# Optimization experiments

Measured on AMD Instinct MI355X. Metric: run time of the kernel, lower is better.

## Reference

```python
import jax, jax.numpy as jnp
import numpy as np

B, T, D_IN, D_OUT = 16, 2048, 2048, 2048
N_ADAPTERS, RANK = 8, 16


def setup_inputs() -> dict:
    key = jax.random.key(0)
    k_x, k_w, k_a, k_b, k_s, k_idx = jax.random.split(key, 6)
    x = jax.random.normal(k_x, (B, T, D_IN), dtype=jnp.float32)
    # frozen base weight (nn.Linear stores W as (d_out, d_in)); bias=False
    W = jax.random.normal(k_w, (D_OUT, D_IN), dtype=jnp.float32) * (1.0 / np.sqrt(D_IN))
    # stacked adapter bank: A[a] is (r, d_in), Bm[a] is (d_out, r)
    A = jax.random.normal(k_a, (N_ADAPTERS, RANK, D_IN), dtype=jnp.float32) * 0.02
    Bm = jax.random.normal(k_b, (N_ADAPTERS, D_OUT, RANK), dtype=jnp.float32) * 0.02
    scalings = jnp.ones((N_ADAPTERS,), dtype=jnp.float32)  # alpha / r, pre-merged
    adapter_idx = jax.random.randint(k_idx, (B,), 0, N_ADAPTERS, dtype=jnp.int32)
    return {"x": x, "W": W, "A": A, "Bm": Bm, "scalings": scalings,
            "adapter_idx": adapter_idx}


def reference(x, W, A, Bm, scalings, adapter_idx):
    # base path: H = x @ W^T   -> (B, T, d_out)
    H = jnp.einsum("btd,od->bto", x, W)
    # per-request adapter gather (replaces the Python loop over adapter groups)
    A_b = A[adapter_idx]          # (B, r, d_in)
    B_b = Bm[adapter_idx]         # (B, d_out, r)
    s_b = scalings[adapter_idx]   # (B,)
    # low-rank delta: (x @ A^T) @ B^T, done per request, fully batched
    xa = jnp.einsum("btd,brd->btr", x, A_b)        # (B, T, r)
    delta = jnp.einsum("btr,bor->bto", xa, B_b)    # (B, T, d_out)
    # original computes delta under torch.no_grad() with detached A/B
    delta = jax.lax.stop_gradient(delta * s_b[:, None, None])
    return H + delta
```

## Files before the change

### kernel.cpp

```cpp
#include <hip/hip_runtime.h>
#include <stdint.h>

typedef unsigned short u16;
typedef __attribute__((ext_vector_type(4))) short s16x4;
typedef __attribute__((ext_vector_type(8))) short short8;
typedef __attribute__((ext_vector_type(4))) float f32x4;

static __device__ __forceinline__ u16 f2bf(float f) {
    union { float f; uint32_t u; } c; c.f = f;
    uint32_t u = c.u;
    u += 0x7FFFu + ((u >> 16) & 1u);
    return (u16)(u >> 16);
}

#define D_IN   2048
#define D_OUT  2048
#define MTOT   32768
#define BK     64
#define NTM    32

__device__ __forceinline__ void gload16(const u16* g, u16* l) {
    __builtin_amdgcn_global_load_lds(
        (const __attribute__((address_space(1))) void*)g,
        (__attribute__((address_space(3))) void*)l, 16, 0, 0);
}

__global__ __launch_bounds__(256) void k_prep(
    const float* __restrict__ W, const float* __restrict__ A, const float* __restrict__ Bm,
    u16* __restrict__ Wb, u16* __restrict__ Ap, u16* __restrict__ Bp)
{
    const int b = blockIdx.x, tid = threadIdx.x;
    if (b < 2048) {
        int i = (b * 256 + tid) * 8;
        const float4* p = (const float4*)(W + i);
        float4 v0 = p[0], v1 = p[1];
        short8 o;
        o[0]=f2bf(v0.x); o[1]=f2bf(v0.y); o[2]=f2bf(v0.z); o[3]=f2bf(v0.w);
        o[4]=f2bf(v1.x); o[5]=f2bf(v1.y); o[6]=f2bf(v1.z); o[7]=f2bf(v1.w);
        *(short8*)(Wb + i) = o;
    } else if (b < 6144) {
        int i = (b - 2048) * 256 + tid;
        int d = i & 2047, r = (i >> 11) & 63, a = i >> 17;
        Ap[i] = (r < 16) ? f2bf(A[(((a << 4) + r) << 11) + d]) : (u16)0;
    } else {
        int i = (b - 6144) * 256 + tid;
        int j = i & 63, n = (i >> 6) & 2047, a = i >> 17;
        Bp[i] = (j < 16) ? f2bf(Bm[((((a << 11) + n)) << 4) + j]) : (u16)0;
    }
}

__global__ __launch_bounds__(256) void k_cast_x_xa(
    const float* __restrict__ x, const u16* __restrict__ Ap,
    const float* __restrict__ scal, const int* __restrict__ aidx,
    u16* __restrict__ xb, u16* __restrict__ xa)
{
    __shared__ __align__(16) u16 Xs[128 * BK];
    __shared__ __align__(16) u16 Ps[64 * BK];
    const int tid = threadIdx.x, lane = tid & 63, wid = tid >> 6;
    const int m0 = blockIdx.x << 7;
    const int a = aidx[m0 >> 11];
    const float s = scal[a];
    const int wr = wid >> 1, wc = wid & 1;
    const int arow = (wr << 6) + (lane & 15);
    const int brow = (wc << 5) + (lane & 15);
    const int scol = ((lane & 7) ^ (lane >> 3)) << 3;

    f32x4 acc[4][2];
    #pragma unroll
    for (int i = 0; i < 4; ++i) { acc[i][0] = 0.f; acc[i][1] = 0.f; }

    const int xrow_l = tid >> 4;
    const int xcol   = (tid & 15) << 2;
    const int wslot  = (tid & 15) >> 1;
    const int wsub   = (tid & 1) << 2;

    const u16* apg = Ap + ((size_t)a << 17);
    const u16* gP[2]; u16* lP[2];
    #pragma unroll
    for (int it = 0; it < 2; ++it) {
        const int chunk = (wid << 1) + it;
        const int row = (chunk << 3) + (lane >> 3);
        gP[it] = apg + ((size_t)row << 11) + scol;
        lP[it] = Ps + (chunk << 9) + (lane << 3);
    }

    for (int kt = 0; kt < NTM; ++kt) {
        const int k0 = kt << 6;
        float4 xv[8];
        #pragma unroll
        for (int r = 0; r < 8; ++r)
            xv[r] = *(const float4*)(x + ((size_t)(m0 + (r << 4) + xrow_l) << 11) + k0 + xcol);
        #pragma unroll
        for (int r = 0; r < 8; ++r) {
            const int row = (r << 4) + xrow_l;
            s16x4 c4;
            c4[0]=f2bf(xv[r].x); c4[1]=f2bf(xv[r].y); c4[2]=f2bf(xv[r].z); c4[3]=f2bf(xv[r].w);
            *(s16x4*)(Xs + (row << 6) + ((wslot ^ (row & 7)) << 3) + wsub) = c4;
            *(s16x4*)(xb + ((size_t)(m0 + row) << 11) + k0 + xcol) = c4;
        }
        gload16(gP[0] + k0, lP[0]);
        gload16(gP[1] + k0, lP[1]);
        asm volatile("s_waitcnt vmcnt(0)" ::: "memory");
        __syncthreads();
        #pragma unroll
        for (int kk = 0; kk < 2; ++kk) {
            const int sl = ((kk << 2) + (lane >> 4)) ^ (lane & 7);
            short8 af[4], bv[2];
            #pragma unroll
            for (int mi = 0; mi < 4; ++mi)
                af[mi] = *(const short8*)(Xs + ((arow + mi * 16) << 6) + (sl << 3));
            #pragma unroll
            for (int ni = 0; ni < 2; ++ni)
                bv[ni] = *(const short8*)(Ps + ((brow + ni * 16) << 6) + (sl << 3));
            #pragma unroll
            for (int mi = 0; mi < 4; ++mi)
                #pragma unroll
                for (int ni = 0; ni < 2; ++ni)
                    acc[mi][ni] = __builtin_amdgcn_mfma_f32_16x16x32_bf16(af[mi], bv[ni], acc[mi][ni], 0, 0, 0);
        }
        __syncthreads();
    }

    #pragma unroll
    for (int mi = 0; mi < 4; ++mi) {
        #pragma unroll
        for (int ni = 0; ni < 2; ++ni) {
            const int cc = (wc << 5) + ni * 16 + (lane & 15);
            #pragma unroll
            for (int rr = 0; rr < 4; ++rr) {
                const int mm = m0 + (wr << 6) + mi * 16 + ((lane >> 4) << 2) + rr;
                xa[((size_t)mm << 6) + cc] = f2bf(acc[mi][ni][rr] * s);
            }
        }
    }
}

__global__ __launch_bounds__(512, 2) void k_gemm(
    const u16* __restrict__ xb, const u16* __restrict__ Wb,
    const u16* __restrict__ xa, const u16* __restrict__ Bp,
    const int* __restrict__ aidx, float* __restrict__ out)
{
    __shared__ __align__(16) u16 LDS[2 * 32768];
    const int tid = threadIdx.x, lane = tid & 63, wid = tid >> 6;

    const int newbid = (blockIdx.x & 7) * 128 + (blockIdx.x >> 3);
    const int bm = newbid >> 3, bn = newbid & 7;
    const int m0 = bm << 8, n0 = bn << 8;
    const int wr = wid >> 2, wc = wid & 3;
    const int a = aidx[m0 >> 11];

    f32x4 acc[8][4];
    #pragma unroll
    for (int i = 0; i < 8; ++i)
        #pragma unroll
        for (int j = 0; j < 4; ++j) acc[i][j] = 0.0f;

    const int sc = ((tid & 7) ^ ((tid >> 3) & 7)) << 3;
    const int srw = tid >> 3;

    const int sl0 = (((lane >> 4)    ) ^ (lane & 7)) << 3;
    const int sl1 = (((lane >> 4) + 4) ^ (lane & 7)) << 3;
    const int aRowBase = (wr << 7) + (lane & 15);
    const int bRowBase = (wc << 6) + (lane & 15);

    short8 af[4][2], bv[4][2];

    auto STG = [&](const u16* ptr, int stride, int rowbase, int kofs, int ldsofs) {
        const u16* s_ = ptr + ((size_t)(rowbase + srw)) * stride + kofs + sc;
        gload16(s_,                          &LDS[ldsofs + (tid << 3)]);
        gload16(s_ + ((size_t)stride << 6),  &LDS[ldsofs + 4096 + (tid << 3)]);
    };
    auto SA = [&](int tt, int h) {
        const int lo = ((tt & 1) << 15) + (h << 13);
        if (tt < NTM) STG(xb, 2048, m0 + (h << 7), tt << 6, lo);
        else          STG(xa, 64,   m0 + (h << 7), 0,       lo);
    };
    auto SB = [&](int tt, int h) {
        const int lo = ((tt & 1) << 15) + 16384 + (h << 13);
        if (tt < NTM) STG(Wb, 2048, n0 + (h << 7), tt << 6, lo);
        else          STG(Bp, 64,   (a << 11) + n0 + (h << 7), 0, lo);
    };

    #define BAR  __builtin_amdgcn_s_barrier()

    #define RDA(c_, mq_) do { _Pragma("unroll")                                     \
        for (int mi = 0; mi < 4; ++mi) {                                            \
            const int row = aRowBase + ((mq_) << 6) + (mi << 4);                    \
            af[mi][0] = *(const short8*)&LDS[((c_) << 15) + (row << 6) + sl0];      \
            af[mi][1] = *(const short8*)&LDS[((c_) << 15) + (row << 6) + sl1];      \
        } } while (0)

    #define RDB(c_, ni_) do {                                                       \
            const int row = bRowBase + ((ni_) << 4);                                \
            bv[ni_][0] = *(const short8*)&LDS[((c_) << 15) + 16384 + (row << 6) + sl0]; \
            bv[ni_][1] = *(const short8*)&LDS[((c_) << 15) + 16384 + (row << 6) + sl1]; \
        } while (0)

    #define MM(mq_, ns_) do { _Pragma("unroll")                                     \
        for (int kk = 0; kk < 2; ++kk) _Pragma("unroll")                            \
        for (int mi = 0; mi < 4; ++mi) _Pragma("unroll")                            \
        for (int j = 0; j < 2; ++j)                                                 \
            acc[(mq_) * 4 + mi][(ns_) * 2 + j] =                                    \
                __builtin_amdgcn_mfma_f32_16x16x32_bf16(af[mi][kk],                 \
                    bv[(ns_) * 2 + j][kk], acc[(mq_) * 4 + mi][(ns_) * 2 + j], 0, 0, 0); \
        } while (0)

    SA(0, 0); SA(0, 1); SB(0, 0); SB(0, 1);

    for (int t = 0; t <= NTM; ++t) {
        const int c = t & 1;
        if (t < NTM) { SA(t + 1, 0); SA(t + 1, 1); SB(t + 1, 0); SB(t + 1, 1); }
        if (t < NTM) asm volatile("s_waitcnt vmcnt(8)" ::: "memory");
        else         asm volatile("s_waitcnt vmcnt(0)" ::: "memory");
        BAR;
        RDB(c, 0); RDB(c, 1); RDA(c, 0);
        MM(0, 0);
        RDB(c, 2); RDB(c, 3);
        MM(0, 1);
        RDA(c, 1);
        MM(1, 0);
        MM(1, 1);
        BAR;
    }

    #undef MM
    #undef RDB
    #undef RDA
    #undef BAR

    #pragma unroll
    for (int mi = 0; mi < 8; ++mi) {
        #pragma unroll
        for (int ni = 0; ni < 4; ++ni) {
            const int nn = n0 + (wc << 6) + ni * 16 + (lane & 15);
            #pragma unroll
            for (int r = 0; r < 4; ++r) {
                const int mm = m0 + (wr << 7) + mi * 16 + ((lane >> 4) << 2) + r;
                out[((size_t)mm << 11) + nn] = acc[mi][ni][r];
            }
        }
    }
}

extern "C" void kernel_launch(void* const* d_in, const int* in_sizes, int n_in,
                              void* d_out, int out_size, void* d_ws, size_t ws_size,
                              hipStream_t stream) {
    const float* x  = (const float*)d_in[0];
    const float* W  = (const float*)d_in[1];
    const float* A  = (const float*)d_in[2];
    const float* Bm = (const float*)d_in[3];
    const float* sc = (const float*)d_in[4];
    const int* aidx = (const int*)d_in[5];
    float* out = (float*)d_out;

    char* ws = (char*)d_ws;
    u16* xb = (u16*)(ws);
    u16* Wb = (u16*)(ws + 134217728);
    u16* Ap = (u16*)(ws + 134217728 + 8388608);
    u16* Bp = (u16*)(ws + 134217728 + 8388608 + 2097152);
    u16* xa = (u16*)(ws + 134217728 + 8388608 + 2097152 + 2097152);

    hipLaunchKernelGGL(k_prep,      dim3(10240), dim3(256), 0, stream, W, A, Bm, Wb, Ap, Bp);
    hipLaunchKernelGGL(k_cast_x_xa, dim3(256),   dim3(256), 0, stream, x, Ap, sc, aidx, xb, xa);
    hipLaunchKernelGGL(k_gemm,      dim3(1024),  dim3(512), 0, stream, xb, Wb, xa, Bp, aidx, out);
}
```

Before: 396.9 us.

## Switch GEMM to 32x32x16 MFMA with fragment-packed operand layouts

```diff
diff --git a/kernel.cpp b/kernel.cpp
--- a/kernel.cpp
+++ b/kernel.cpp
@@ -5,6 +5,7 @@
 typedef __attribute__((ext_vector_type(4))) short s16x4;
 typedef __attribute__((ext_vector_type(8))) short short8;
 typedef __attribute__((ext_vector_type(4))) float f32x4;
+typedef __attribute__((ext_vector_type(16))) float f32x16;
 
 static __device__ __forceinline__ u16 f2bf(float f) {
     union { float f; uint32_t u; } c; c.f = f;
@@ -18,6 +19,7 @@
 #define MTOT   32768
 #define BK     64
 #define NTM    32
+
 
 __device__ __forceinline__ void gload16(const u16* g, u16* l) {
     __builtin_amdgcn_global_load_lds(
@@ -32,12 +34,15 @@
     const int b = blockIdx.x, tid = threadIdx.x;
     if (b < 2048) {
         int i = (b * 256 + tid) * 8;
+        int n = i >> 11, c = i & 2047;
         const float4* p = (const float4*)(W + i);
         float4 v0 = p[0], v1 = p[1];
         short8 o;
         o[0]=f2bf(v0.x); o[1]=f2bf(v0.y); o[2]=f2bf(v0.z); o[3]=f2bf(v0.w);
         o[4]=f2bf(v1.x); o[5]=f2bf(v1.y); o[6]=f2bf(v1.z); o[7]=f2bf(v1.w);
-        *(short8*)(Wb + i) = o;
+        const int np = n >> 8, kt = c >> 6, nb = (n & 255) >> 5, ks = (c >> 4) & 3;
+        const int lane = (n & 31) + (((c >> 3) & 1) << 5);
+        *(short8*)(Wb + (((size_t)(np << 5) + kt) << 14) + (((nb << 2) + ks) << 9) + (lane << 3)) = o;
     } else if (b < 6144) {
         int i = (b - 2048) * 256 + tid;
         int d = i & 2047, r = (i >> 11) & 63, a = i >> 17;
@@ -45,7 +50,10 @@
     } else {
         int i = (b - 6144) * 256 + tid;
         int j = i & 63, n = (i >> 6) & 2047, a = i >> 17;
-        Bp[i] = (j < 16) ? f2bf(Bm[((((a << 11) + n)) << 4) + j]) : (u16)0;
+        float v = (j < 16) ? Bm[((((a << 11) + n)) << 4) + j] : 0.0f;
+        const int np = n >> 8, nb = (n & 255) >> 5, ks = j >> 4;
+        const int lane = (n & 31) + (((j >> 3) & 1) << 5), sub = j & 7;
+        Bp[((size_t)a << 17) + ((size_t)np << 14) + (((nb << 2) + ks) << 9) + (lane << 3) + sub] = f2bf(v);
     }
 }
 
@@ -129,7 +137,11 @@
             #pragma unroll
             for (int rr = 0; rr < 4; ++rr) {
                 const int mm = m0 + (wr << 6) + mi * 16 + ((lane >> 4) << 2) + rr;
-                xa[((size_t)mm << 6) + cc] = f2bf(acc[mi][ni][rr] * s);
+                const int p = mm >> 8, r = mm & 255;
+                const int mb = r >> 5, ks = cc >> 4;
+                const int fl = (r & 31) + (((cc >> 3) & 1) << 5), sub = cc & 7;
+                xa[((size_t)p << 14) + (((mb << 2) + ks) << 9) + (fl << 3) + sub] =
+                    f2bf(acc[mi][ni][rr] * s);
             }
         }
     }
@@ -149,94 +161,102 @@
     const int wr = wid >> 2, wc = wid & 3;
     const int a = aidx[m0 >> 11];
 
-    f32x4 acc[8][4];
-    #pragma unroll
-    for (int i = 0; i < 8; ++i)
-        #pragma unroll
-        for (int j = 0; j < 4; ++j) acc[i][j] = 0.0f;
-
-    const int sc = ((tid & 7) ^ ((tid >> 3) & 7)) << 3;
-    const int srw = tid >> 3;
-
-    const int sl0 = (((lane >> 4)    ) ^ (lane & 7)) << 3;
-    const int sl1 = (((lane >> 4) + 4) ^ (lane & 7)) << 3;
-    const int aRowBase = (wr << 7) + (lane & 15);
-    const int bRowBase = (wc << 6) + (lane & 15);
-
-    short8 af[4][2], bv[4][2];
-
-    auto STG = [&](const u16* ptr, int stride, int rowbase, int kofs, int ldsofs) {
-        const u16* s_ = ptr + ((size_t)(rowbase + srw)) * stride + kofs + sc;
-        gload16(s_,                          &LDS[ldsofs + (tid << 3)]);
-        gload16(s_ + ((size_t)stride << 6),  &LDS[ldsofs + 4096 + (tid << 3)]);
-    };
-    auto SA = [&](int tt, int h) {
-        const int lo = ((tt & 1) << 15) + (h << 13);
-        if (tt < NTM) STG(xb, 2048, m0 + (h << 7), tt << 6, lo);
-        else          STG(xa, 64,   m0 + (h << 7), 0,       lo);
-    };
-    auto SB = [&](int tt, int h) {
-        const int lo = ((tt & 1) << 15) + 16384 + (h << 13);
-        if (tt < NTM) STG(Wb, 2048, n0 + (h << 7), tt << 6, lo);
-        else          STG(Bp, 64,   (a << 11) + n0 + (h << 7), 0, lo);
-    };
-
-    #define BAR  __builtin_amdgcn_s_barrier()
-
-    #define RDA(c_, mq_) do { _Pragma("unroll")                                     \
-        for (int mi = 0; mi < 4; ++mi) {                                            \
-            const int row = aRowBase + ((mq_) << 6) + (mi << 4);                    \
-            af[mi][0] = *(const short8*)&LDS[((c_) << 15) + (row << 6) + sl0];      \
-            af[mi][1] = *(const short8*)&LDS[((c_) << 15) + (row << 6) + sl1];      \
+    f32x16 acc[4][2];
+    #pragma unroll
+    for (int i = 0; i < 4; ++i)
+        #pragma unroll
+        for (int j = 0; j < 2; ++j)
+            #pragma unroll
+            for (int r = 0; r < 16; ++r) acc[i][j][r] = 0.0f;
+
+    const u16* sA = xb + ((size_t)(m0 + (wid << 5) + (lane & 31)) << 11) + ((lane >> 5) << 3);
+    const u16* sB = Wb + ((size_t)(bn << 5) << 14) + ((wid << 2) << 9) + (lane << 3);
+    const u16* sTA = xa + ((size_t)(m0 >> 8) << 14) + ((wid << 2) << 9) + (lane << 3);
+    const u16* sTB = Bp + ((size_t)a << 17) + ((size_t)bn << 14) + ((wid << 2) << 9) + (lane << 3);
+    u16* dA = &LDS[((wid << 2) << 9) + (lane << 3)];
+    u16* dB = &LDS[16384 + ((wid << 2) << 9) + (lane << 3)];
+
+    #define STAGE(tt, bb) do {                                                      \
+        if ((tt) < NTM) {                                                           \
+            const u16* a_ = sA + ((tt) << 6);                                       \
+            _Pragma("unroll")                                                       \
+            for (int j = 0; j < 4; ++j) gload16(a_ + (j << 4), dA + ((bb) << 15) + (j << 9)); \
+            const u16* b_ = sB + ((size_t)(tt) << 14);                              \
+            _Pragma("unroll")                                                       \
+            for (int j = 0; j < 4; ++j) gload16(b_ + (j << 9), dB + ((bb) << 15) + (j << 9)); \
+        } else {                                                                    \
+            _Pragma("unroll")                                                       \
+            for (int j = 0; j < 4; ++j) gload16(sTA + (j << 9), dA + ((bb) << 15) + (j << 9)); \
+            _Pragma("unroll")                                                       \
+            for (int j = 0; j < 4; ++j) gload16(sTB + (j << 9), dB + ((bb) << 15) + (j << 9)); \
         } } while (0)
 
-    #define RDB(c_, ni_) do {                                                       \
-            const int row = bRowBase + ((ni_) << 4);                                \
-            bv[ni_][0] = *(const short8*)&LDS[((c_) << 15) + 16384 + (row << 6) + sl0]; \
-            bv[ni_][1] = *(const short8*)&LDS[((c_) << 15) + 16384 + (row << 6) + sl1]; \
+    short8 afP[4], bvP[2], afQ[4], bvQ[2];
+
+    #define RD(S, c_, ks_) do { _Pragma("unroll")                                   \
+        for (int mi = 0; mi < 4; ++mi)                                              \
+            af##S[mi] = *(const short8*)&LDS[((c_) << 15) +                         \
+                (((wr << 4) + (mi << 2) + (ks_)) << 9) + (lane << 3)];              \
+        _Pragma("unroll")                                                           \
+        for (int i = 0; i < 2; ++i)                                                 \
+            bv##S[i] = *(const short8*)&LDS[((c_) << 15) + 16384 +                  \
+                (((wc << 3) + (i << 2) + (ks_)) << 9) + (lane << 3)];               \
         } while (0)
 
-    #define MM(mq_, ns_) do { _Pragma("unroll")                                     \
-        for (int kk = 0; kk < 2; ++kk) _Pragma("unroll")                            \
+    #define BAR __builtin_amdgcn_s_barrier()
+    #define VM0 asm volatile("s_waitcnt vmcnt(0)" ::: "memory")
+    #define LGK(n) do { asm volatile("s_waitcnt lgkmcnt(" #n ")" ::: "memory");     \
+                        __builtin_amdgcn_sched_barrier(0); } while (0)
+
+    #define MM(S) do { __builtin_amdgcn_s_setprio(1); _Pragma("unroll")             \
         for (int mi = 0; mi < 4; ++mi) _Pragma("unroll")                            \
-        for (int j = 0; j < 2; ++j)                                                 \
-            acc[(mq_) * 4 + mi][(ns_) * 2 + j] =                                    \
-                __builtin_amdgcn_mfma_f32_16x16x32_bf16(af[mi][kk],                 \
-                    bv[(ns_) * 2 + j][kk], acc[(mq_) * 4 + mi][(ns_) * 2 + j], 0, 0, 0); \
-        } while (0)
-
-    SA(0, 0); SA(0, 1); SB(0, 0); SB(0, 1);
+        for (int i = 0; i < 2; ++i)                                                 \
+            acc[mi][i] = __builtin_amdgcn_mfma_f32_32x32x16_bf16(                   \
+                af##S[mi], bv##S[i], acc[mi][i], 0, 0, 0);                          \
+        __builtin_amdgcn_s_setprio(0); } while (0)
+
+    STAGE(0, 0);
+    VM0;
+    BAR;
+    RD(P, 0, 0);
 
     for (int t = 0; t <= NTM; ++t) {
-        const int c = t & 1;
-        if (t < NTM) { SA(t + 1, 0); SA(t + 1, 1); SB(t + 1, 0); SB(t + 1, 1); }
-        if (t < NTM) asm volatile("s_waitcnt vmcnt(8)" ::: "memory");
-        else         asm volatile("s_waitcnt vmcnt(0)" ::: "memory");
-        BAR;
-        RDB(c, 0); RDB(c, 1); RDA(c, 0);
-        MM(0, 0);
-        RDB(c, 2); RDB(c, 3);
-        MM(0, 1);
-        RDA(c, 1);
-        MM(1, 0);
-        MM(1, 1);
-        BAR;
+        const int c = t & 1, cn = c ^ 1;
+        RD(Q, c, 1);
+        if (t < NTM) STAGE(t + 1, cn);
+        LGK(6); MM(P);
+        RD(P, c, 2);
+        LGK(6); MM(Q);
+        RD(Q, c, 3);
+        LGK(6); MM(P);
+        if (t < NTM) {
+            VM0; BAR;
+            RD(P, cn, 0);
+            LGK(6); MM(Q);
+            BAR;
+        } else {
+            LGK(0); MM(Q);
+        }
     }
 
     #undef MM
-    #undef RDB
-    #undef RDA
+    #undef LGK
+    #undef VM0
     #undef BAR
-
-    #pragma unroll
-    for (int mi = 0; mi < 8; ++mi) {
-        #pragma unroll
-        for (int ni = 0; ni < 4; ++ni) {
-            const int nn = n0 + (wc << 6) + ni * 16 + (lane & 15);
-            #pragma unroll
-            for (int r = 0; r < 4; ++r) {
-                const int mm = m0 + (wr << 7) + mi * 16 + ((lane >> 4) << 2) + r;
-                out[((size_t)mm << 11) + nn] = acc[mi][ni][r];
+    #undef RD
+    #undef STAGE
+
+    const int l31 = lane & 31, h5 = lane >> 5;
+    #pragma unroll
+    for (int mi = 0; mi < 4; ++mi) {
+        #pragma unroll
+        for (int i = 0; i < 2; ++i) {
+            const int nn = n0 + (wc << 6) + (i << 5) + l31;
+            #pragma unroll
+            for (int r = 0; r < 16; ++r) {
+                const int row = (r & 3) + ((r >> 2) << 3) + (h5 << 2);
+                const int mm = m0 + (wr << 7) + (mi << 5) + row;
+                out[((size_t)mm << 11) + nn] = acc[mi][i][r];
             }
         }
     }
```

Result: slower. 458.6 us (+15.5%).
